# Performance work log

Hardware: AMD Instinct MI355X
Metric: run time of the kernel (lower is better)

Reference implementation:

```python
import jax, jax.numpy as jnp
import numpy as np

B, C, N, MAX_OUT = 8, 80, 8192, 100


def setup_inputs() -> dict:
    key = jax.random.key(0)
    k1, k2, k3 = jax.random.split(key, 3)
    xy = jax.random.uniform(k1, (B, N, 2), dtype=jnp.float32)          # top-left corners in [0,1)
    wh = jax.random.uniform(k2, (B, N, 2), dtype=jnp.float32,
                            minval=0.01, maxval=0.2)                    # realistic box sizes
    boxes = jnp.concatenate([xy, xy + wh], axis=-1)                     # [B,N,4] xyxy
    scores = jax.random.uniform(k3, (B, C, N), dtype=jnp.float32)       # [B,C,N]
    return {
        "boxes": boxes,
        "scores": scores,
        "max_output_boxes_per_class": MAX_OUT,
        "iou_threshold": jnp.array([0.5], dtype=jnp.float32),
        "score_threshold": jnp.array([0.5], dtype=jnp.float32),
    }


def _nms_single(boxes, scores, iou_thr, score_thr, max_out):
    """Greedy NMS for one (batch, class): boxes [N,4] xyxy, scores [N].
    Returns [max_out] selected box indices, padded with -1."""
    n = scores.shape[0]
    x1, y1, x2, y2 = boxes[:, 0], boxes[:, 1], boxes[:, 2], boxes[:, 3]
    area = jnp.maximum(x2 - x1, 0.0) * jnp.maximum(y2 - y1, 0.0)
    # score filtering (strictly greater, as in the torch module)
    s0 = jnp.where(scores > score_thr, scores, -jnp.inf)
    iota = jnp.arange(n)

    def body(s, _):
        i = jnp.argmax(s)
        valid = s[i] > -jnp.inf
        bx1, by1, bx2, by2 = boxes[i, 0], boxes[i, 1], boxes[i, 2], boxes[i, 3]
        iw = jnp.maximum(jnp.minimum(x2, bx2) - jnp.maximum(x1, bx1), 0.0)
        ih = jnp.maximum(jnp.minimum(y2, by2) - jnp.maximum(y1, by1), 0.0)
        inter = iw * ih
        union = area + area[i] - inter
        iou = jnp.where(union > 0, inter / union, 0.0)
        # suppress overlapping boxes (iou > thr keeps iou <= thr, matching torchvision.ops.nms)
        suppress = (iou > iou_thr) | (iota == i)
        s_new = jnp.where(suppress, -jnp.inf, s)
        s = jnp.where(valid, s_new, s)
        return s, jnp.where(valid, i, -1)

    _, idxs = jax.lax.scan(body, s0, None, length=max_out)
    return idxs  # [max_out] int32, -1 padded


def reference(boxes, scores, max_output_boxes_per_class, iou_threshold, score_threshold):
    max_out = int(max_output_boxes_per_class)
    iou_thr = iou_threshold[0]
    score_thr = score_threshold[0]
    b, c = scores.shape[0], scores.shape[1]

    # vmap over classes (boxes shared), then over batch
    per_batch = jax.vmap(
        lambda bb, ss: jax.vmap(
            lambda s: _nms_single(bb, s, iou_thr, score_thr, max_out)
        )(ss)
    )
    idxs = per_batch(boxes, scores)  # [B,C,max_out], -1 padded

    valid = idxs >= 0
    bidx = jnp.broadcast_to(jnp.arange(b)[:, None, None], idxs.shape)
    cidx = jnp.broadcast_to(jnp.arange(c)[None, :, None], idxs.shape)
    # [B*C*max_out, 3] rows of (batch, class, box_index); padded rows are (-1,-1,-1).
    triplets = jnp.stack(
        [jnp.where(valid, bidx, -1), jnp.where(valid, cidx, -1), idxs], axis=-1
    ).reshape(-1, 3).astype(jnp.int64)
    return triplets
```

## Files before the change

### kernel.cpp

```cpp
#include <hip/hip_runtime.h>
#include <math.h>
#include <stdint.h>

#define NMS_B 8
#define NMS_C 80
#define NMS_N 8192
#define NMS_MAX_OUT 100
#define BLOCK 512
#define PT 16
#define NBINS 256
#define TARGET 192
#define CAP 256
#define KTOP 192
#define NW 3
#define PADROWS 8

__global__ __launch_bounds__(BLOCK) void nms_k192_kernel(
    const float4* __restrict__ boxes,
    const float*  __restrict__ scores,
    const float*  __restrict__ iou_thr_p,
    const float*  __restrict__ score_thr_p,
    int32_t* __restrict__ out)
{
    const int bc   = blockIdx.x;
    const int b    = bc / NMS_C;
    const int c    = bc % NMS_C;
    const int t    = threadIdx.x;
    const int lane = t & 63;
    const int wv   = t >> 6;

    const float iou_thr   = *iou_thr_p;
    const float score_thr = *score_thr_p;

    const uint32_t tu  = __float_as_uint(iou_thr);
    const float  tsucc = __uint_as_float(tu + 1u);
    const double md    = 0.5 * ((double)iou_thr + (double)tsucc);
    const bool tie_up  = (tu & 1u) != 0u;
    const bool zgt     = (0.0f > iou_thr);

    __shared__ int      hist[NBINS];
    __shared__ int      cut_bin;
    __shared__ int      gcount;
    __shared__ alignas(16) uint64_t ckey[CAP];
    __shared__ float4   cbox[CAP];
    __shared__ int      cidx[CAP];
    __shared__ float4   sbox[CAP + PADROWS];
    __shared__ float    sar[CAP + PADROWS];
    __shared__ int      sidx[CAP];
    __shared__ int      rnk0[CAP], rnk1[CAP];
    __shared__ alignas(16) uint64_t adjT[KTOP * NW];

    if (t < NBINS) { hist[t] = 0; ckey[t] = 0; }
    for (int i = t; i < CAP + PADROWS; i += BLOCK) {
        sbox[i] = make_float4(0.0f, 0.0f, 0.0f, 0.0f);
        sar[i]  = 0.0f;
    }
    if (t < (KTOP * NW) / 2) {
        ulonglong2 z; z.x = 0; z.y = 0;
        ((ulonglong2*)adjT)[t] = z;
    }
    if (t == 0) { cut_bin = 0; gcount = 0; }
    __syncthreads();

    const float* ss = scores + ((size_t)b * NMS_C + c) * NMS_N;
    const float4* ssv = (const float4*)ss;
    float s[PT];
    #pragma unroll
    for (int k4 = 0; k4 < PT / 4; ++k4) {
        float4 v = ssv[k4 * BLOCK + t];
        s[4 * k4 + 0] = v.x; s[4 * k4 + 1] = v.y;
        s[4 * k4 + 2] = v.z; s[4 * k4 + 3] = v.w;
    }
    const float inv_range =
        (score_thr < 1.0f) ? (float)NBINS / (1.0f - score_thr) : 0.0f;
    uint32_t pk[PT / 4] = {0, 0, 0, 0};
    #pragma unroll
    for (int k = 0; k < PT; ++k) {
        if (s[k] > score_thr) {
            int bin = (int)((s[k] - score_thr) * inv_range);
            bin = bin > NBINS - 1 ? NBINS - 1 : bin;
            atomicAdd(&hist[bin], 1);
            pk[k >> 2] |= (uint32_t)bin << ((k & 3) * 8);
        }
    }
    __syncthreads();

    if (wv == 0) {
        int h0 = hist[lane], h1 = hist[64 + lane];
        int h2 = hist[128 + lane], h3 = hist[192 + lane];
        #pragma unroll
        for (int off = 1; off < 64; off <<= 1) {
            const int o0 = __shfl_down(h0, off);
            const int o1 = __shfl_down(h1, off);
            const int o2 = __shfl_down(h2, off);
            const int o3 = __shfl_down(h3, off);
            if (lane + off < 64) { h0 += o0; h1 += o1; h2 += o2; h3 += o3; }
        }
        const int tot1 = __shfl(h1, 0);
        const int tot2 = __shfl(h2, 0);
        const int tot3 = __shfl(h3, 0);
        const int S3 = h3;
        const int S2 = h2 + tot3;
        const int S1 = h1 + tot2 + tot3;
        const int S0 = h0 + tot1 + tot2 + tot3;
        const unsigned long long q3 = __ballot(S3 >= TARGET);
        const unsigned long long q2 = __ballot(S2 >= TARGET);
        const unsigned long long q1 = __ballot(S1 >= TARGET);
        const unsigned long long q0 = __ballot(S0 >= TARGET);
        int cut = 0;
        if      (q3) cut = 192 + 63 - __clzll(q3);
        else if (q2) cut = 128 + 63 - __clzll(q2);
        else if (q1) cut = 64  + 63 - __clzll(q1);
        else if (q0) cut = 63 - __clzll(q0);
        if (lane == 0) cut_bin = cut;
    }
    __syncthreads();
    const int cb = cut_bin;

    const float4* bb = boxes + (size_t)b * NMS_N;
    #pragma unroll
    for (int k = 0; k < PT; ++k) {
        if (s[k] > score_thr) {
            const int bin = (pk[k >> 2] >> ((k & 3) * 8)) & 255;
            if (bin >= cb) {
                int pos = atomicAdd(&gcount, 1);
                if (pos < CAP) {
                    const int k4 = k >> 2, el = k & 3;
                    const int idx = (k4 * BLOCK + t) * 4 + el;
                    cbox[pos] = bb[idx];
                    cidx[pos] = idx;
                    ckey[pos] = ((uint64_t)__float_as_uint(s[k]) << 32) |
                                (uint32_t)(NMS_N - idx);
                }
            }
        }
    }
    __syncthreads();
    const int M    = gcount < CAP ? gcount : CAP;
    const int Keff = M < KTOP ? M : KTOP;

    {
        const int key_id = t & 255;
        const int half   = t >> 8;
        const uint64_t mykey = ckey[key_id];
        const ulonglong2* kp = ((const ulonglong2*)ckey) + half * (CAP / 4);
        int r = 0;
        #pragma unroll 8
        for (int k = 0; k < CAP / 4; ++k) {
            const ulonglong2 kk = kp[k];
            r += (kk.x > mykey) ? 1 : 0;
            r += (kk.y > mykey) ? 1 : 0;
        }
        if (half) rnk1[key_id] = r; else rnk0[key_id] = r;
    }
    __syncthreads();

    if (t < CAP) {
        const uint64_t mykey = ckey[t];
        if (mykey != 0) {
            const int r = rnk0[t] + rnk1[t];
            const float4 v = cbox[t];
            sbox[r] = v;
            sar[r]  = fmaxf(v.z - v.x, 0.0f) * fmaxf(v.w - v.y, 0.0f);
            sidx[r] = cidx[t];
        }
    }
    __syncthreads();

    {
        const int L0c = Keff <  64 ? Keff :  64;
        const int L1c = Keff < 128 ? Keff : 128;
        const int L2c = Keff;
        int cum[4];
        cum[0] = 0;
        cum[1] = L0c;
        cum[2] = L0c + L1c;
        cum[3] = L0c + L1c + L2c;
        const int G  = cum[3];
        const int g0 = ((wv * G) >> 3) & ~3;
        const int g1 = (wv == 7) ? G : (((wv + 1) * G) >> 3) & ~3;

        for (int cw = 0; cw < 3; ++cw) {
            const int a = g0 > cum[cw] ? g0 : cum[cw];
            const int e = g1 < cum[cw + 1] ? g1 : cum[cw + 1];
            if (a >= e) continue;
            const int rlo = (a - cum[cw]) & ~3;
            const int rhi = e - cum[cw];
            const int col = cw * 64 + lane;
            const float4 cb4  = sbox[col];
            const float carea = sar[col];

            int cur_word = rlo >> 6;
            uint64_t acc = 0;
            float4 p0 = sbox[rlo + 0], p1 = sbox[rlo + 1];
            float4 p2 = sbox[rlo + 2], p3 = sbox[rlo + 3];

            for (int i = rlo; i < rhi; i += 4) {
                const int wblk = i >> 6;
                if (wblk != cur_word) {
                    if (acc) atomicOr(
                        (unsigned long long*)&adjT[col * NW + cur_word],
                        (unsigned long long)acc);
                    acc = 0; cur_word = wblk;
                }
                const float4 q0 = p0, q1 = p1, q2 = p2, q3 = p3;
                p0 = sbox[i + 4]; p1 = sbox[i + 5];
                p2 = sbox[i + 6]; p3 = sbox[i + 7];
                #pragma unroll
                for (int u = 0; u < 4; ++u) {
                    const float4 r4 = (u == 0) ? q0 : (u == 1) ? q1
                                     : (u == 2) ? q2 : q3;
                    const int row = i + u;
                    const float rarea = (r4.z - r4.x) * (r4.w - r4.y);
                    const float iw =
                        fmaxf(fminf(cb4.z, r4.z) - fmaxf(cb4.x, r4.x), 0.0f);
                    const float ih =
                        fmaxf(fminf(cb4.w, r4.w) - fmaxf(cb4.y, r4.y), 0.0f);
                    const float inter = iw * ih;
                    const float uni   = carea + rarea - inter;
                    const double di = (double)inter;
                    const double dx = (double)uni * md;
                    const bool qcmp = tie_up ? (di >= dx) : (di > dx);
                    const bool sup  = (uni > 0.0f) ? qcmp : zgt;
                    const uint64_t bit = (sup && row < rhi) ? 1ull : 0ull;
                    acc |= bit << (row & 63);
                }
            }
            if (acc) atomicOr(
                (unsigned long long*)&adjT[col * NW + cur_word],
                (unsigned long long)acc);
        }
    }
    __syncthreads();

    int32_t* o = out + (size_t)bc * NMS_MAX_OUT * 3;
    if (t >= 64) return;

    uint64_t adj_[3][3];
    #pragma unroll
    for (int w2 = 0; w2 < 3; ++w2) {
        const int col = w2 * 64 + lane;
        adj_[w2][0] = adjT[col * NW + 0];
        adj_[w2][1] = adjT[col * NW + 1];
        adj_[w2][2] = adjT[col * NW + 2];
    }
    uint64_t V[3];
    #pragma unroll
    for (int ww = 0; ww < 3; ++ww) {
        const int rem = Keff - ww * 64;
        V[ww] = (rem >= 64) ? ~0ull : (rem > 0 ? ((1ull << rem) - 1) : 0ull);
    }
    uint64_t A0 = V[0], A1 = V[1], A2 = V[2];
    const uint64_t lanelow = (1ull << lane) - 1;

    for (int iter = 0; iter <= KTOP; ++iter) {
        bool acc[3];
        #pragma unroll
        for (int w2 = 0; w2 < 3; ++w2) {
            uint64_t rem = 0;
            const uint64_t Aw[3] = {A0, A1, A2};
            #pragma unroll
            for (int ww = 0; ww < 3; ++ww) {
                const uint64_t lm = (ww < w2) ? ~0ull
                                  : (ww == w2 ? lanelow : 0ull);
                rem |= Aw[ww] & lm & adj_[w2][ww];
            }
            acc[w2] = (((V[w2] >> lane) & 1ull) != 0) && (rem == 0);
        }
        const uint64_t N0 = __ballot(acc[0]);
        const uint64_t N1 = __ballot(acc[1]);
        const uint64_t N2 = __ballot(acc[2]);
        const bool same = (N0 == A0) && (N1 == A1) && (N2 == A2);
        A0 = N0; A1 = N1; A2 = N2;
        if (same) break;
    }

    const int pc0 = __popcll(A0), pc1 = __popcll(A1), pc2 = __popcll(A2);
    const int total = pc0 + pc1 + pc2;
    const int nacc = total < NMS_MAX_OUT ? total : NMS_MAX_OUT;
    const int base[3] = {0, pc0, pc0 + pc1};
    #pragma unroll
    for (int w2 = 0; w2 < 3; ++w2) {
        const uint64_t Aw = (w2 == 0) ? A0 : (w2 == 1) ? A1 : A2;
        if ((Aw >> lane) & 1ull) {
            const int rank = base[w2] + __popcll(Aw & lanelow);
            if (rank < NMS_MAX_OUT) {
                const int col = w2 * 64 + lane;
                o[rank * 3 + 0] = b;
                o[rank * 3 + 1] = c;
                o[rank * 3 + 2] = sidx[col];
            }
        }
    }
    for (int m = nacc + t; m < NMS_MAX_OUT; m += 64) {
        o[m * 3 + 0] = -1;
        o[m * 3 + 1] = -1;
        o[m * 3 + 2] = -1;
    }
}

extern "C" void kernel_launch(void* const* d_in, const int* in_sizes, int n_in,
                              void* d_out, int out_size, void* d_ws, size_t ws_size,
                              hipStream_t stream) {
    (void)in_sizes; (void)n_in; (void)d_ws; (void)ws_size; (void)out_size;
    const float4* boxes  = (const float4*)d_in[0];
    const float*  scores = (const float*)d_in[1];
    const float*  iou_thr   = (const float*)d_in[3];
    const float*  score_thr = (const float*)d_in[4];
    int32_t* out = (int32_t*)d_out;

    dim3 grid(NMS_B * NMS_C);
    dim3 block(BLOCK);
    hipLaunchKernelGGL(nms_k192_kernel, grid, block, 0, stream,
                       boxes, scores, iou_thr, score_thr, out);
}
```

Baseline: 99.85 us.

## Add fast 128-candidate NMS path with 192-candidate fallback

Builds the IoU adjacency matrix and runs the fixed-point greedy resolution on only the top 128 candidates first. When that yields at least 100 kept boxes, or there are no more candidates, it writes output and exits. Otherwise it computes the third column block and reruns over 192 candidates. It also drops a barrier by having every wave compute the histogram cut redundantly. This removes roughly half of the pairwise IoU work in the common case, at the cost of extra work and a barrier when the fallback triggers.

Result: faster. 94.36 us (-5.5%).

```diff
diff --git a/kernel.cpp b/kernel.cpp
--- a/kernel.cpp
+++ b/kernel.cpp
@@ -12,10 +12,11 @@
 #define TARGET 192
 #define CAP 256
 #define KTOP 192
+#define KFAST 128
 #define NW 3
 #define PADROWS 8
 
-__global__ __launch_bounds__(BLOCK) void nms_k192_kernel(
+__global__ __launch_bounds__(BLOCK) void nms_fastfb_kernel(
     const float4* __restrict__ boxes,
     const float*  __restrict__ scores,
     const float*  __restrict__ iou_thr_p,
@@ -39,8 +40,8 @@
     const bool zgt     = (0.0f > iou_thr);
 
     __shared__ int      hist[NBINS];
-    __shared__ int      cut_bin;
     __shared__ int      gcount;
+    __shared__ int      need_fb;
     __shared__ alignas(16) uint64_t ckey[CAP];
     __shared__ float4   cbox[CAP];
     __shared__ int      cidx[CAP];
@@ -59,7 +60,7 @@
         ulonglong2 z; z.x = 0; z.y = 0;
         ((ulonglong2*)adjT)[t] = z;
     }
-    if (t == 0) { cut_bin = 0; gcount = 0; }
+    if (t == 0) gcount = 0;
     __syncthreads();
 
     const float* ss = scores + ((size_t)b * NMS_C + c) * NMS_N;
@@ -85,7 +86,8 @@
     }
     __syncthreads();
 
-    if (wv == 0) {
+    int cut;
+    {
         int h0 = hist[lane], h1 = hist[64 + lane];
         int h2 = hist[128 + lane], h3 = hist[192 + lane];
         #pragma unroll
@@ -107,22 +109,19 @@
         const unsigned long long q2 = __ballot(S2 >= TARGET);
         const unsigned long long q1 = __ballot(S1 >= TARGET);
         const unsigned long long q0 = __ballot(S0 >= TARGET);
-        int cut = 0;
+        cut = 0;
         if      (q3) cut = 192 + 63 - __clzll(q3);
         else if (q2) cut = 128 + 63 - __clzll(q2);
         else if (q1) cut = 64  + 63 - __clzll(q1);
         else if (q0) cut = 63 - __clzll(q0);
-        if (lane == 0) cut_bin = cut;
-    }
-    __syncthreads();
-    const int cb = cut_bin;
+    }
 
     const float4* bb = boxes + (size_t)b * NMS_N;
     #pragma unroll
     for (int k = 0; k < PT; ++k) {
         if (s[k] > score_thr) {
             const int bin = (pk[k >> 2] >> ((k & 3) * 8)) & 255;
-            if (bin >= cb) {
+            if (bin >= cut) {
                 int pos = atomicAdd(&gcount, 1);
                 if (pos < CAP) {
                     const int k4 = k >> 2, el = k & 3;
@@ -136,8 +135,9 @@
         }
     }
     __syncthreads();
-    const int M    = gcount < CAP ? gcount : CAP;
-    const int Keff = M < KTOP ? M : KTOP;
+    const int M     = gcount < CAP ? gcount : CAP;
+    const int Keff2 = M < KFAST ? M : KFAST;
+    const int Keff3 = M < KTOP ? M : KTOP;
 
     {
         const int key_id = t & 255;
@@ -168,19 +168,15 @@
     __syncthreads();
 
     {
-        const int L0c = Keff <  64 ? Keff :  64;
-        const int L1c = Keff < 128 ? Keff : 128;
-        const int L2c = Keff;
-        int cum[4];
-        cum[0] = 0;
-        cum[1] = L0c;
-        cum[2] = L0c + L1c;
-        cum[3] = L0c + L1c + L2c;
-        const int G  = cum[3];
+        const int L0c = Keff2 < 64 ? Keff2 : 64;
+        const int L1c = Keff2;
+        int cum[3];
+        cum[0] = 0; cum[1] = L0c; cum[2] = L0c + L1c;
+        const int G  = cum[2];
         const int g0 = ((wv * G) >> 3) & ~3;
         const int g1 = (wv == 7) ? G : (((wv + 1) * G) >> 3) & ~3;
 
-        for (int cw = 0; cw < 3; ++cw) {
+        for (int cw = 0; cw < 2; ++cw) {
             const int a = g0 > cum[cw] ? g0 : cum[cw];
             const int e = g1 < cum[cw + 1] ? g1 : cum[cw + 1];
             if (a >= e) continue;
@@ -220,8 +216,8 @@
                     const float uni   = carea + rarea - inter;
                     const double di = (double)inter;
                     const double dx = (double)uni * md;
-                    const bool qcmp = tie_up ? (di >= dx) : (di > dx);
-                    const bool sup  = (uni > 0.0f) ? qcmp : zgt;
+                    const bool qc  = tie_up ? (di >= dx) : (di > dx);
+                    const bool sup = (uni > 0.0f) ? qc : zgt;
                     const uint64_t bit = (sup && row < rhi) ? 1ull : 0ull;
                     acc |= bit << (row & 63);
                 }
@@ -234,68 +230,171 @@
     __syncthreads();
 
     int32_t* o = out + (size_t)bc * NMS_MAX_OUT * 3;
+    const uint64_t lanelow = (1ull << lane) - 1;
+
+    uint64_t A0 = 0, A1 = 0;
+    if (t < 64) {
+        const uint64_t a00 = adjT[lane * NW + 0];
+        const uint64_t a10 = adjT[(64 + lane) * NW + 0];
+        const uint64_t a11 = adjT[(64 + lane) * NW + 1];
+        const int rem0 = Keff2;
+        const int rem1 = Keff2 - 64;
+        const uint64_t V0 = (rem0 >= 64) ? ~0ull
+                          : (rem0 > 0 ? ((1ull << rem0) - 1) : 0ull);
+        const uint64_t V1 = (rem1 >= 64) ? ~0ull
+                          : (rem1 > 0 ? ((1ull << rem1) - 1) : 0ull);
+        const bool v0 = ((V0 >> lane) & 1ull) != 0;
+        const bool v1 = ((V1 >> lane) & 1ull) != 0;
+        A0 = V0; A1 = V1;
+        for (int iter = 0; iter <= KFAST; ++iter) {
+            const bool acc0 = v0 && ((A0 & lanelow & a00) == 0);
+            const bool acc1 = v1 &&
+                (((A0 & a10) | (A1 & lanelow & a11)) == 0);
+            const uint64_t N0 = __ballot(acc0);
+            const uint64_t N1 = __ballot(acc1);
+            const bool same = (N0 == A0) && (N1 == A1);
+            A0 = N0; A1 = N1;
+            if (same) break;
+        }
+        const int total = __popcll(A0) + __popcll(A1);
+        const bool ok = (total >= NMS_MAX_OUT) || (M <= KFAST);
+        if (t == 0) need_fb = ok ? 0 : 1;
+    }
+    __syncthreads();
+
+    if (!need_fb) {
+        if (t < 64) {
+            const int pc0 = __popcll(A0), pc1 = __popcll(A1);
+            const int total = pc0 + pc1;
+            const int nacc = total < NMS_MAX_OUT ? total : NMS_MAX_OUT;
+            if ((A0 >> lane) & 1ull) {
+                const int rank = __popcll(A0 & lanelow);
+                if (rank < NMS_MAX_OUT) {
+                    o[rank * 3 + 0] = b;
+                    o[rank * 3 + 1] = c;
+                    o[rank * 3 + 2] = sidx[lane];
+                }
+            }
+            if ((A1 >> lane) & 1ull) {
+                const int rank = pc0 + __popcll(A1 & lanelow);
+                if (rank < NMS_MAX_OUT) {
+                    o[rank * 3 + 0] = b;
+                    o[rank * 3 + 1] = c;
+                    o[rank * 3 + 2] = sidx[64 + lane];
+                }
+            }
+            for (int m = nacc + t; m < NMS_MAX_OUT; m += 64) {
+                o[m * 3 + 0] = -1;
+                o[m * 3 + 1] = -1;
+                o[m * 3 + 2] = -1;
+            }
+        }
+        return;
+    }
+
+    {
+        const int rlo = ((wv * Keff3) >> 3) & ~3;
+        const int rhi = (wv == 7) ? Keff3 : (((wv + 1) * Keff3) >> 3) & ~3;
+        if (rlo < rhi) {
+            const int col = 128 + lane;
+            const float4 cb4  = sbox[col];
+            const float carea = sar[col];
+            int cur_word = rlo >> 6;
+            uint64_t acc = 0;
+            float4 p0 = sbox[rlo + 0], p1 = sbox[rlo + 1];
+            float4 p2 = sbox[rlo + 2], p3 = sbox[rlo + 3];
+            for (int i = rlo; i < rhi; i += 4) {
+                const int wblk = i >> 6;
+                if (wblk != cur_word) {
+                    if (acc) atomicOr(
+                        (unsigned long long*)&adjT[col * NW + cur_word],
+                        (unsigned long long)acc);
+                    acc = 0; cur_word = wblk;
+                }
+                const float4 q0 = p0, q1 = p1, q2 = p2, q3 = p3;
+                p0 = sbox[i + 4]; p1 = sbox[i + 5];
+                p2 = sbox[i + 6]; p3 = sbox[i + 7];
+                #pragma unroll
+                for (int u = 0; u < 4; ++u) {
+                    const float4 r4 = (u == 0) ? q0 : (u == 1) ? q1
+                                     : (u == 2) ? q2 : q3;
+                    const int row = i + u;
+                    const float rarea = (r4.z - r4.x) * (r4.w - r4.y);
+                    const float iw =
+                        fmaxf(fminf(cb4.z, r4.z) - fmaxf(cb4.x, r4.x), 0.0f);
+                    const float ih =
+                        fmaxf(fminf(cb4.w, r4.w) - fmaxf(cb4.y, r4.y), 0.0f);
+                    const float inter = iw * ih;
+                    const float uni   = carea + rarea - inter;
+                    const double di = (double)inter;
+                    const double dx = (double)uni * md;
+                    const bool qc  = tie_up ? (di >= dx) : (di > dx);
+                    const bool sup = (uni > 0.0f) ? qc : zgt;
+                    const uint64_t bit = (sup && row < rhi) ? 1ull : 0ull;
+                    acc |= bit << (row & 63);
+                }
+            }
+            if (acc) atomicOr(
+                (unsigned long long*)&adjT[col * NW + cur_word],
+                (unsigned long long)acc);
+        }
+    }
+    __syncthreads();
     if (t >= 64) return;
 
-    uint64_t adj_[3][3];
-    #pragma unroll
-    for (int w2 = 0; w2 < 3; ++w2) {
-        const int col = w2 * 64 + lane;
-        adj_[w2][0] = adjT[col * NW + 0];
-        adj_[w2][1] = adjT[col * NW + 1];
-        adj_[w2][2] = adjT[col * NW + 2];
-    }
-    uint64_t V[3];
-    #pragma unroll
-    for (int ww = 0; ww < 3; ++ww) {
-        const int rem = Keff - ww * 64;
-        V[ww] = (rem >= 64) ? ~0ull : (rem > 0 ? ((1ull << rem) - 1) : 0ull);
-    }
-    uint64_t A0 = V[0], A1 = V[1], A2 = V[2];
-    const uint64_t lanelow = (1ull << lane) - 1;
-
-    for (int iter = 0; iter <= KTOP; ++iter) {
-        bool acc[3];
+    {
+        const uint64_t a00 = adjT[lane * NW + 0];
+        const uint64_t a10 = adjT[(64 + lane) * NW + 0];
+        const uint64_t a11 = adjT[(64 + lane) * NW + 1];
+        const uint64_t a20 = adjT[(128 + lane) * NW + 0];
+        const uint64_t a21 = adjT[(128 + lane) * NW + 1];
+        const uint64_t a22 = adjT[(128 + lane) * NW + 2];
+        uint64_t V[3];
+        #pragma unroll
+        for (int ww = 0; ww < 3; ++ww) {
+            const int rem = Keff3 - ww * 64;
+            V[ww] = (rem >= 64) ? ~0ull
+                  : (rem > 0 ? ((1ull << rem) - 1) : 0ull);
+        }
+        const bool v0 = ((V[0] >> lane) & 1ull) != 0;
+        const bool v1 = ((V[1] >> lane) & 1ull) != 0;
+        const bool v2 = ((V[2] >> lane) & 1ull) != 0;
+        uint64_t B0 = V[0], B1 = V[1], B2 = V[2];
+        for (int iter = 0; iter <= KTOP; ++iter) {
+            const bool acc0 = v0 && ((B0 & lanelow & a00) == 0);
+            const bool acc1 = v1 &&
+                (((B0 & a10) | (B1 & lanelow & a11)) == 0);
+            const bool acc2 = v2 &&
+                (((B0 & a20) | (B1 & a21) | (B2 & lanelow & a22)) == 0);
+            const uint64_t N0 = __ballot(acc0);
+            const uint64_t N1 = __ballot(acc1);
+            const uint64_t N2 = __ballot(acc2);
+            const bool same = (N0 == B0) && (N1 == B1) && (N2 == B2);
+            B0 = N0; B1 = N1; B2 = N2;
+            if (same) break;
+        }
+        const int pc0 = __popcll(B0), pc1 = __popcll(B1), pc2 = __popcll(B2);
+        const int total = pc0 + pc1 + pc2;
+        const int nacc = total < NMS_MAX_OUT ? total : NMS_MAX_OUT;
+        const int base[3] = {0, pc0, pc0 + pc1};
         #pragma unroll
         for (int w2 = 0; w2 < 3; ++w2) {
-            uint64_t rem = 0;
-            const uint64_t Aw[3] = {A0, A1, A2};
-            #pragma unroll
-            for (int ww = 0; ww < 3; ++ww) {
-                const uint64_t lm = (ww < w2) ? ~0ull
-                                  : (ww == w2 ? lanelow : 0ull);
-                rem |= Aw[ww] & lm & adj_[w2][ww];
-            }
-            acc[w2] = (((V[w2] >> lane) & 1ull) != 0) && (rem == 0);
-        }
-        const uint64_t N0 = __ballot(acc[0]);
-        const uint64_t N1 = __ballot(acc[1]);
-        const uint64_t N2 = __ballot(acc[2]);
-        const bool same = (N0 == A0) && (N1 == A1) && (N2 == A2);
-        A0 = N0; A1 = N1; A2 = N2;
-        if (same) break;
-    }
-
-    const int pc0 = __popcll(A0), pc1 = __popcll(A1), pc2 = __popcll(A2);
-    const int total = pc0 + pc1 + pc2;
-    const int nacc = total < NMS_MAX_OUT ? total : NMS_MAX_OUT;
-    const int base[3] = {0, pc0, pc0 + pc1};
-    #pragma unroll
-    for (int w2 = 0; w2 < 3; ++w2) {
-        const uint64_t Aw = (w2 == 0) ? A0 : (w2 == 1) ? A1 : A2;
-        if ((Aw >> lane) & 1ull) {
-            const int rank = base[w2] + __popcll(Aw & lanelow);
-            if (rank < NMS_MAX_OUT) {
-                const int col = w2 * 64 + lane;
-                o[rank * 3 + 0] = b;
-                o[rank * 3 + 1] = c;
-                o[rank * 3 + 2] = sidx[col];
-            }
-        }
-    }
-    for (int m = nacc + t; m < NMS_MAX_OUT; m += 64) {
-        o[m * 3 + 0] = -1;
-        o[m * 3 + 1] = -1;
-        o[m * 3 + 2] = -1;
+            const uint64_t Aw = (w2 == 0) ? B0 : (w2 == 1) ? B1 : B2;
+            if ((Aw >> lane) & 1ull) {
+                const int rank = base[w2] + __popcll(Aw & lanelow);
+                if (rank < NMS_MAX_OUT) {
+                    const int col = w2 * 64 + lane;
+                    o[rank * 3 + 0] = b;
+                    o[rank * 3 + 1] = c;
+                    o[rank * 3 + 2] = sidx[col];
+                }
+            }
+        }
+        for (int m = nacc + t; m < NMS_MAX_OUT; m += 64) {
+            o[m * 3 + 0] = -1;
+            o[m * 3 + 1] = -1;
+            o[m * 3 + 2] = -1;
+        }
     }
 }
 
@@ -311,6 +410,6 @@
 
     dim3 grid(NMS_B * NMS_C);
     dim3 block(BLOCK);
-    hipLaunchKernelGGL(nms_k192_kernel, grid, block, 0, stream,
+    hipLaunchKernelGGL(nms_fastfb_kernel, grid, block, 0, stream,
                        boxes, scores, iou_thr, score_thr, out);
 }
```
